# Kernel optimization log

Measured on AMD Instinct MI355X. Metric: run time of the kernel, lower is better.

## Reference

```python
import jax, jax.numpy as jnp
import numpy as np

EMBED_DIM = 1024
NUM_HEADS = 16
SEQ_LEN = 2048
BATCH = 2
LN_EPS = 1e-5


def setup_inputs() -> dict:
    key = jax.random.key(0)
    ks = jax.random.split(key, 12)
    d = EMBED_DIM
    s = 1.0 / np.sqrt(d)
    inp = {
        "x": jax.random.normal(ks[0], (BATCH, SEQ_LEN, d), dtype=jnp.float32),
        "ln1_g": jnp.ones((d,), jnp.float32),
        "ln1_b": jnp.zeros((d,), jnp.float32),
        "ln2_g": jnp.ones((d,), jnp.float32),
        "ln2_b": jnp.zeros((d,), jnp.float32),
        "W_qkv": jax.random.normal(ks[1], (d, 3 * d), jnp.float32) * s,
        "b_qkv": jnp.zeros((3 * d,), jnp.float32),
        "W_proj": jax.random.normal(ks[2], (d, d), jnp.float32) * s,
        "b_proj": jnp.zeros((d,), jnp.float32),
        "W_fc": jax.random.normal(ks[3], (d, 4 * d), jnp.float32) * s,
        "b_fc": jnp.zeros((4 * d,), jnp.float32),
        "W_out": jax.random.normal(ks[4], (4 * d, d), jnpp_dummy := jnp.float32) * (1.0 / np.sqrt(4 * d)),
        "b_out": jnp.zeros((d,), jnp.float32),
    }
    return inp


def _layernorm(x, g, b):
    mu = jnp.mean(x, axis=-1, keepdims=True)
    var = jnp.mean(jnp.square(x - mu), axis=-1, keepdims=True)
    return (x - mu) * jax.lax.rsqrt(var + LN_EPS) * g + b


def _block(x, ln1_g, ln1_b, ln2_g, ln2_b, W_qkv, b_qkv, W_proj, b_proj, W_fc, b_fc, W_out, b_out):
    B, S, D = x.shape
    H = NUM_HEADS
    hd = D // H
    h = _layernorm(x, ln1_g, ln1_b)
    qkv = h @ W_qkv + b_qkv  # [B,S,3D]
    q, k, v = jnp.split(qkv, 3, axis=-1)
    # [B,H,S,hd]
    q = q.reshape(B, S, H, hd).transpose(0, 2, 1, 3)
    k = k.reshape(B, S, H, hd).transpose(0, 2, 1, 3)
    v = v.reshape(B, S, H, hd).transpose(0, 2, 1, 3)
    attn = jnp.einsum("bhqd,bhkd->bhqk", q, k) / np.sqrt(hd).astype(np.float32)
    causal = jnp.tril(jnp.ones((S, S), dtype=bool))
    attn = jnp.where(causal, attn, -jnp.inf)
    attn = jax.nn.softmax(attn, axis=-1)
    y = jnp.einsum("bhqk,bhkd->bhqd", attn, v)
    y = y.transpose(0, 2, 1, 3).reshape(B, S, D)
    y = y @ W_proj + b_proj
    x = x + y
    h2 = _layernorm(x, ln2_g, ln2_b)
    m = jax.nn.relu(h2 @ W_fc + b_fc) @ W_out + b_out
    return x + m


def reference(x, ln1_g, ln1_b, ln2_g, ln2_b, W_qkv, b_qkv, W_proj, b_proj, W_fc, b_fc, W_out, b_out):
    return _block(x, ln1_g, ln1_b, ln2_g, ln2_b, W_qkv, b_qkv, W_proj, b_proj, W_fc, b_fc, W_out, b_out)
```

## Files before the change

kernel.cpp:

```cpp
#include <hip/hip_runtime.h>

typedef unsigned short u16;
typedef __attribute__((ext_vector_type(8))) __bf16 bf16x8;
typedef __attribute__((ext_vector_type(4))) float f32x4;

#define DEV __device__ __forceinline__

DEV u16 f2bf(float f) {
  unsigned u = __float_as_uint(f);
  u += 0x7fffu + ((u >> 16) & 1u);
  return (u16)(u >> 16);
}
DEV float bf2f(u16 u) { return __uint_as_float((unsigned)u << 16); }

DEV void gl_lds16(const void* g, void* l) {
  __builtin_amdgcn_global_load_lds(
      (const __attribute__((address_space(1))) void*)(uintptr_t)g,
      (__attribute__((address_space(3))) void*)(unsigned)(uintptr_t)l, 16, 0, 0);
}

DEV float wave_sum64(float v) {
#pragma unroll
  for (int off = 32; off > 0; off >>= 1) v += __shfl_down(v, off);
  return v;
}

DEV void ln_body(const float4 v, const float* g, const float* be, u16* out_row, int t,
                 float* red) {
  const int w = t >> 6, L = t & 63;
  float s = v.x + v.y + v.z + v.w;
  s = wave_sum64(s);
  if (L == 0) red[w] = s;
  __syncthreads();
  const float mean = (red[0] + red[1] + red[2] + red[3]) * (1.0f / 1024.0f);
  const float dx = v.x - mean, dy = v.y - mean, dz = v.z - mean, dw = v.w - mean;
  float q = dx * dx + dy * dy + dz * dz + dw * dw;
  q = wave_sum64(q);
  if (L == 0) red[4 + w] = q;
  __syncthreads();
  const float var = (red[4] + red[5] + red[6] + red[7]) * (1.0f / 1024.0f);
  const float rs = rsqrtf(var + 1e-5f);
  const float4 gg = reinterpret_cast<const float4*>(g)[t];
  const float4 bb = reinterpret_cast<const float4*>(be)[t];
  ushort4 o;
  o.x = f2bf(dx * rs * gg.x + bb.x);
  o.y = f2bf(dy * rs * gg.y + bb.y);
  o.z = f2bf(dz * rs * gg.z + bb.z);
  o.w = f2bf(dw * rs * gg.w + bb.w);
  reinterpret_cast<ushort4*>(out_row)[t] = o;
}

__global__ __launch_bounds__(256) void prep_kernel(
    const float* __restrict__ x, const float* __restrict__ ln1g,
    const float* __restrict__ ln1b, u16* __restrict__ hbuf,
    const float* __restrict__ Wqkv, u16* __restrict__ wt_qkv,
    const float* __restrict__ Wproj, u16* __restrict__ wt_proj,
    const float* __restrict__ Wfc, u16* __restrict__ wt_fc,
    const float* __restrict__ Wout, u16* __restrict__ wt_out) {
  __shared__ float smem[32 * 33];
  int id = blockIdx.x;
  const int t = threadIdx.x;
  if (id < 4096) {
    const float4 v = reinterpret_cast<const float4*>(x + (size_t)id * 1024)[t];
    ln_body(v, ln1g, ln1b, hbuf + (size_t)id * 1024, t, smem);
    return;
  }
  id -= 4096;
  const float* W;
  u16* Wt;
  int K, N, nbx;
  if (id < 3072) {
    W = Wqkv; Wt = wt_qkv; K = 1024; N = 3072; nbx = 96;
  } else if (id < 3072 + 1024) {
    id -= 3072; W = Wproj; Wt = wt_proj; K = 1024; N = 1024; nbx = 32;
  } else if (id < 3072 + 1024 + 4096) {
    id -= 3072 + 1024; W = Wfc; Wt = wt_fc; K = 1024; N = 4096; nbx = 128;
  } else {
    id -= 3072 + 1024 + 4096; W = Wout; Wt = wt_out; K = 4096; N = 1024; nbx = 32;
  }
  float(*tile)[33] = (float(*)[33])smem;
  const int c0 = (id % nbx) * 32, r0 = (id / nbx) * 32;
  const int tx = t & 31, ty = t >> 5;
#pragma unroll
  for (int j = 0; j < 4; ++j)
    tile[ty + j * 8][tx] = W[(size_t)(r0 + ty + j * 8) * N + c0 + tx];
  __syncthreads();
#pragma unroll
  for (int j = 0; j < 4; ++j) {
    const int n = c0 + ty + j * 8, k = r0 + tx;
    Wt[(size_t)n * K + k] = f2bf(tile[tx][ty + j * 8]);
  }
}

__global__ __launch_bounds__(256) void proj_reduce_ln(const float* __restrict__ x,
                                                      const float* __restrict__ bias,
                                                      const u16* __restrict__ P0,
                                                      const u16* __restrict__ P1,
                                                      const float* __restrict__ g,
                                                      const float* __restrict__ be,
                                                      float* __restrict__ x2,
                                                      u16* __restrict__ hbuf) {
  const int row = blockIdx.x, t = threadIdx.x;
  const size_t off = (size_t)row * 1024;
  __shared__ float red[8];
  const float4 xv = reinterpret_cast<const float4*>(x + off)[t];
  const float4 bv = reinterpret_cast<const float4*>(bias)[t];
  const ushort4 p0 = reinterpret_cast<const ushort4*>(P0 + off)[t];
  const ushort4 p1 = reinterpret_cast<const ushort4*>(P1 + off)[t];
  float4 v;
  v.x = xv.x + bv.x + bf2f(p0.x) + bf2f(p1.x);
  v.y = xv.y + bv.y + bf2f(p0.y) + bf2f(p1.y);
  v.z = xv.z + bv.z + bf2f(p0.z) + bf2f(p1.z);
  v.w = xv.w + bv.w + bf2f(p0.w) + bf2f(p1.w);
  reinterpret_cast<float4*>(x2 + off)[t] = v;
  ln_body(v, g, be, hbuf + off, t, red);
}

__global__ __launch_bounds__(256) void out_reduce(const float* __restrict__ x2,
                                                  const float* __restrict__ bias,
                                                  const u16* __restrict__ P0,
                                                  const u16* __restrict__ P1,
                                                  const u16* __restrict__ P2,
                                                  const u16* __restrict__ P3,
                                                  float* __restrict__ dout) {
  const int row = blockIdx.x, t = threadIdx.x;
  const size_t off = (size_t)row * 1024;
  const float4 xv = reinterpret_cast<const float4*>(x2 + off)[t];
  const float4 bv = reinterpret_cast<const float4*>(bias)[t];
  const ushort4 a = reinterpret_cast<const ushort4*>(P0 + off)[t];
  const ushort4 b = reinterpret_cast<const ushort4*>(P1 + off)[t];
  const ushort4 c = reinterpret_cast<const ushort4*>(P2 + off)[t];
  const ushort4 d = reinterpret_cast<const ushort4*>(P3 + off)[t];
  float4 o;
  o.x = xv.x + bv.x + bf2f(a.x) + bf2f(b.x) + bf2f(c.x) + bf2f(d.x);
  o.y = xv.y + bv.y + bf2f(a.y) + bf2f(b.y) + bf2f(c.y) + bf2f(d.y);
  o.z = xv.z + bv.z + bf2f(a.z) + bf2f(b.z) + bf2f(c.z) + bf2f(d.z);
  o.w = xv.w + bv.w + bf2f(a.w) + bf2f(b.w) + bf2f(c.w) + bf2f(d.w);
  reinterpret_cast<float4*>(dout + off)[t] = o;
}

enum { F_BIAS = 1, F_RESID = 2, F_RELU = 4, F_BF16 = 8, F_PART4 = 32, F_VT = 64 };

template <int FLAGS>
__global__ __launch_bounds__(256, 2) void gemm_bt(const u16* __restrict__ A,
                                                  const u16* __restrict__ Bt,
                                                  const float* __restrict__ bias,
                                                  const float* __restrict__ resid,
                                                  void* __restrict__ Cout,
                                                  u16* __restrict__ pp0, u16* __restrict__ pp1,
                                                  u16* __restrict__ pp2, u16* __restrict__ pp3,
                                                  int M, int N, int K, int Kst) {
  __shared__ __attribute__((aligned(16))) u16 sA[2][128 * 32];
  __shared__ __attribute__((aligned(16))) u16 sB[2][128 * 32];

  const int gx = gridDim.x, gy = gridDim.y;
  const int tilesPerZ = gx * gy;
  int lin = (blockIdx.z * gy + blockIdx.y) * gx + blockIdx.x;
  const int total = tilesPerZ * gridDim.z;
  if (!(total & 7)) lin = (lin & 7) * (total >> 3) + (lin >> 3);
  const int zz = lin / tilesPerZ;
  const int pid = lin - zz * tilesPerZ;
  const int npg = gx << 3;
  const int gid = pid / npg;
  const int rem = pid - gid * npg;
  const int fm = gid << 3;
  const int gsm = (gy - fm < 8) ? (gy - fm) : 8;
  const int bm = fm + rem % gsm;
  const int bn = rem / gsm;

  const int t = threadIdx.x, w = t >> 6, L = t & 63, quad = L >> 4, l15 = L & 15;
  const int wm = w >> 1, wn = w & 1;
  const int m0 = bm * 128, n0 = bn * 128;
  const u16* Ag = A + (size_t)m0 * Kst + (size_t)zz * K;
  const u16* Bg = Bt + (size_t)n0 * Kst + (size_t)zz * K;

  f32x4 acc[4][4] = {};

  for (int k0 = 0; k0 < K; k0 += 64) {
    __syncthreads();
#pragma unroll
    for (int h = 0; h < 2; ++h) {
#pragma unroll
      for (int i = 0; i < 2; ++i) {
        const int cp = i * 256 + t, rr = cp >> 2, cc = (cp & 3) << 3;
        gl_lds16(Ag + (size_t)rr * Kst + k0 + h * 32 + cc, &sA[h][(i * 256 + w * 64) * 8]);
      }
#pragma unroll
      for (int i = 0; i < 2; ++i) {
        const int cp = i * 256 + t, rr = cp >> 2, cc = (cp & 3) << 3;
        gl_lds16(Bg + (size_t)rr * Kst + k0 + h * 32 + cc, &sB[h][(i * 256 + w * 64) * 8]);
      }
    }
    __syncthreads();

#pragma unroll
    for (int h = 0; h < 2; ++h) {
      bf16x8 af[4], bfr[4];
#pragma unroll
      for (int m = 0; m < 4; ++m)
        af[m] = *(const bf16x8*)&sA[h][(wm * 64 + m * 16 + l15) * 32 + quad * 8];
#pragma unroll
      for (int n = 0; n < 4; ++n)
        bfr[n] = *(const bf16x8*)&sB[h][(wn * 64 + n * 16 + l15) * 32 + quad * 8];
#pragma unroll
      for (int m = 0; m < 4; ++m)
#pragma unroll
        for (int n = 0; n < 4; ++n)
          acc[m][n] =
              __builtin_amdgcn_mfma_f32_16x16x32_bf16(af[m], bfr[n], acc[m][n], 0, 0, 0);
    }
  }

  if ((FLAGS & F_VT) && n0 >= 2048) {
#pragma unroll
    for (int m = 0; m < 4; ++m) {
#pragma unroll
      for (int n = 0; n < 4; ++n) {
        const int col = n0 + wn * 64 + n * 16 + l15;
        const float bv = bias[col];
        const int hh = (col - 2048) >> 6, dd = col & 63;
        const int srow = m0 + wm * 64 + m * 16 + quad * 4;
        const int bb = srow >> 11, ss = srow & 2047;
        ushort4 tmp;
        tmp.x = f2bf(acc[m][n][0] + bv);
        tmp.y = f2bf(acc[m][n][1] + bv);
        tmp.z = f2bf(acc[m][n][2] + bv);
        tmp.w = f2bf(acc[m][n][3] + bv);
        *(ushort4*)(pp0 + ((size_t)((bb * 16 + hh) * 64 + dd)) * 2048 + ss) = tmp;
      }
    }
    return;
  }

  u16* pbase = nullptr;
  if (FLAGS & F_PART4)
    pbase = (zz == 0) ? pp0 : (zz == 1) ? pp1 : (zz == 2) ? pp2 : pp3;

#pragma unroll
  for (int m = 0; m < 4; ++m) {
#pragma unroll
    for (int n = 0; n < 4; ++n) {
      const int col = n0 + wn * 64 + n * 16 + l15;
      const float bv = (FLAGS & F_BIAS) ? bias[col] : 0.0f;
#pragma unroll
      for (int rr = 0; rr < 4; ++rr) {
        const int row = m0 + wm * 64 + m * 16 + quad * 4 + rr;
        if (FLAGS & F_PART4) {
          pbase[(size_t)row * N + col] = f2bf(acc[m][n][rr]);
        } else {
          float v = acc[m][n][rr] + bv;
          if (FLAGS & F_RESID) v += resid[(size_t)row * N + col];
          if (FLAGS & F_RELU) v = fmaxf(v, 0.0f);
          if (FLAGS & F_BF16)
            ((u16*)Cout)[(size_t)row * N + col] = f2bf(v);
          else
            ((float*)Cout)[(size_t)row * N + col] = v;
        }
      }
    }
  }
}

__global__ __launch_bounds__(512) void flash_attn(const u16* __restrict__ qkv,
                                                  const u16* __restrict__ Vt,
                                                  u16* __restrict__ y,
                                                  float* __restrict__ acc0,
                                                  float* __restrict__ acc1,
                                                  float* __restrict__ lacc0,
                                                  float* __restrict__ lacc1) {
  constexpr int S = 2048, D3 = 3072, D = 1024;
  constexpr float Csc = 0.125f * 1.44269504088896f;
  __shared__ __attribute__((aligned(16))) u16 sK[64 * 64];
  __shared__ __attribute__((aligned(16))) u16 sV[64 * 64];
  __shared__ __attribute__((aligned(16))) u16 sP[8][2 * 16 * 40];

  const int bid = blockIdx.x;
  const int bh = bid & 31;
  const int e = bid >> 5;
  int qt, it0, it1, part;
  if (e < 8) {
    qt = 8 + e; it0 = 0; it1 = 16; part = 1;
  } else {
    const int j = (e - 8) >> 1;
    if (((e - 8) & 1) == 0) {
      qt = 7 - j; it0 = 0; it1 = 2 * qt + 2; part = 0;
    } else {
      qt = 15 - j; it0 = 16; it1 = 2 * qt + 2; part = 2;
    }
  }
  const int b = bh >> 4, h = bh & 15;
  const int q0 = qt * 128;

  const int t = threadIdx.x, w = t >> 6, L = t & 63, quad = L >> 4, l15 = L & 15;
  const int qw = q0 + w * 16;

  const u16* qbase = qkv + (size_t)(b * S) * D3 + h * 64;
  const u16* Kbase = qbase + D;
  const u16* Vbase = Vt + (size_t)((b * 16 + h) * 64) * S;

  const int srow = t >> 3;
  const int k8 = ((t & 7) ^ (srow & 7)) << 3;
  const u16* Ksrc = Kbase + (size_t)srow * D3 + k8;
  const u16* Vsrc = Vbase + (size_t)srow * S + k8;
  u16* sKdst = &sK[(w * 64) * 8];
  u16* sVdst = &sV[(w * 64) * 8];

  bf16x8 aQ[2];
#pragma unroll
  for (int kk = 0; kk < 2; ++kk)
    aQ[kk] = *(const bf16x8*)(qbase + (size_t)(qw + l15) * D3 + kk * 32 + quad * 8);

  bf16x8 ones;
#pragma unroll
  for (int i = 0; i < 8; ++i) ones[i] = (__bf16)1.0f;

  f32x4 acc[4] = {};
  f32x4 lacc = {};

  u16* sPw = sP[w];
  const int swz = l15 & 7;

  gl_lds16(Ksrc + (size_t)(it0 * 64) * D3, sKdst);
  gl_lds16(Vsrc + it0 * 64, sVdst);

  for (int it = it0; it < it1; ++it) {
    const int kv0 = it * 64;
    asm volatile("s_waitcnt vmcnt(0)" ::: "memory");
    __builtin_amdgcn_s_barrier();

    f32x4 s[4] = {};
    __builtin_amdgcn_s_setprio(1);
#pragma unroll
    for (int kk = 0; kk < 2; ++kk) {
#pragma unroll
      for (int n = 0; n < 4; ++n) {
        const bf16x8 bK =
            *(const bf16x8*)&sK[(n * 16 + l15) * 64 + ((kk * 4 + quad) ^ swz) * 8];
        s[n] = __builtin_amdgcn_mfma_f32_16x16x32_bf16(aQ[kk], bK, s[n], 0, 0, 0);
      }
    }
    __builtin_amdgcn_s_setprio(0);

    if (kv0 + 63 > qw) {
#pragma unroll
      for (int n = 0; n < 4; ++n) {
        const int col = kv0 + n * 16 + l15;
#pragma unroll
        for (int r = 0; r < 4; ++r) {
          const int row = qw + quad * 4 + r;
          const float p = __builtin_amdgcn_exp2f(s[n][r] * Csc);
          s[n][r] = (col > row) ? 0.0f : p;
        }
      }
    } else {
#pragma unroll
      for (int n = 0; n < 4; ++n)
#pragma unroll
        for (int r = 0; r < 4; ++r) s[n][r] = __builtin_amdgcn_exp2f(s[n][r] * Csc);
    }

#pragma unroll
    for (int n = 0; n < 4; ++n)
#pragma unroll
      for (int r = 0; r < 4; ++r)
        sPw[(n >> 1) * 640 + (quad * 4 + r) * 40 + (n & 1) * 16 + l15] = f2bf(s[n][r]);

    __builtin_amdgcn_s_setprio(1);
#pragma unroll
    for (int kk = 0; kk < 2; ++kk) {
      const bf16x8 aP = *(const bf16x8*)&sPw[kk * 640 + l15 * 40 + quad * 8];
      lacc = __builtin_amdgcn_mfma_f32_16x16x32_bf16(aP, ones, lacc, 0, 0, 0);
#pragma unroll
      for (int dn = 0; dn < 4; ++dn) {
        const bf16x8 bV =
            *(const bf16x8*)&sV[(dn * 16 + l15) * 64 + ((kk * 4 + quad) ^ swz) * 8];
        acc[dn] = __builtin_amdgcn_mfma_f32_16x16x32_bf16(aP, bV, acc[dn], 0, 0, 0);
      }
    }
    __builtin_amdgcn_s_setprio(0);

    asm volatile("s_waitcnt lgkmcnt(0)" ::: "memory");
    __builtin_amdgcn_s_barrier();
    if (it + 1 < it1) {
      const int kvn = kv0 + 64;
      gl_lds16(Ksrc + (size_t)kvn * D3, sKdst);
      gl_lds16(Vsrc + kvn, sVdst);
    }
  }

  if (part == 0) {
#pragma unroll
    for (int r = 0; r < 4; ++r) {
      const float inv = 1.0f / lacc[r];
      const int row = qw + quad * 4 + r;
      u16* yb = y + (size_t)(b * S + row) * D + h * 64 + l15;
#pragma unroll
      for (int dn = 0; dn < 4; ++dn) yb[dn * 16] = f2bf(acc[dn][r] * inv);
    }
  } else {
    float* accP = (part == 1) ? acc0 : acc1;
    float* laccP = (part == 1) ? lacc0 : lacc1;
#pragma unroll
    for (int r = 0; r < 4; ++r) {
      const int row = qw + quad * 4 + r;
      const int g = (bh << 10) + (row - 1024);
      float* ap = accP + (size_t)g * 64 + l15;
#pragma unroll
      for (int dn = 0; dn < 4; ++dn) ap[dn * 16] = acc[dn][r];
      if (l15 == 0) laccP[g] = lacc[r];
    }
  }
}

__global__ __launch_bounds__(256) void attn_combine(const float* __restrict__ acc0,
                                                    const float* __restrict__ acc1,
                                                    const float* __restrict__ lacc0,
                                                    const float* __restrict__ lacc1,
                                                    u16* __restrict__ y) {
  const int t = threadIdx.x;
  const int g = blockIdx.x * 4 + (t >> 6);
  const int d = t & 63;
  const int bh = g >> 10, ri = g & 1023;
  const int b = bh >> 4, h = bh & 15;
  const int row = 1024 + ri;
  const size_t po = (size_t)g * 64 + d;
  const float l = lacc0[g] + lacc1[g];
  const float v = (acc0[po] + acc1[po]) / l;
  y[((size_t)(b * 2048 + row)) * 1024 + h * 64 + d] = f2bf(v);
}

extern "C" void kernel_launch(void* const* d_in, const int* in_sizes, int n_in,
                              void* d_out, int out_size, void* d_ws, size_t ws_size,
                              hipStream_t stream) {
  const float* x = (const float*)d_in[0];
  const float* ln1g = (const float*)d_in[1];
  const float* ln1b = (const float*)d_in[2];
  const float* ln2g = (const float*)d_in[3];
  const float* ln2b = (const float*)d_in[4];
  const float* Wqkv = (const float*)d_in[5];
  const float* bqkv = (const float*)d_in[6];
  const float* Wproj = (const float*)d_in[7];
  const float* bproj = (const float*)d_in[8];
  const float* Wfc = (const float*)d_in[9];
  const float* bfc = (const float*)d_in[10];
  const float* Wout = (const float*)d_in[11];
  const float* bout = (const float*)d_in[12];

  char* ws = (char*)d_ws;
  const size_t MB = 1u << 20;
  u16* wt_out = (u16*)(ws + 0 * MB);
  u16* hbuf = (u16*)(ws + 8 * MB);
  float* x2 = (float*)(ws + 16 * MB);
  u16* ybuf = (u16*)(ws + 32 * MB);
  u16* qkvb = (u16*)(ws + 40 * MB);
  u16* vtb = (u16*)(ws + 64 * MB);
  u16* wt_qkv = (u16*)(ws + 72 * MB);
  u16* wt_proj = (u16*)(ws + 78 * MB);
  u16* wt_fc = (u16*)(ws + 80 * MB);
  u16* projP0 = (u16*)(ws + 40 * MB);
  u16* projP1 = (u16*)(ws + 48 * MB);
  u16* m1 = (u16*)(ws + 40 * MB);
  u16* po0 = (u16*)(ws + 8 * MB);
  u16* po1 = (u16*)(ws + 32 * MB);
  u16* po2 = (u16*)(ws + 72 * MB);
  u16* po3 = (u16*)(ws + 80 * MB);
  float* facc0 = (float*)(ws + 8 * MB);
  float* facc1 = (float*)(ws + 16 * MB);
  float* flacc0 = (float*)(ws + 24 * MB);
  float* flacc1 = (float*)(ws + 25 * MB);

  prep_kernel<<<4096 + 3072 + 1024 + 4096 + 4096, 256, 0, stream>>>(
      x, ln1g, ln1b, hbuf, Wqkv, wt_qkv, Wproj, wt_proj, Wfc, wt_fc, Wout, wt_out);

  gemm_bt<F_BIAS | F_BF16 | F_VT><<<dim3(24, 32), 256, 0, stream>>>(
      hbuf, wt_qkv, bqkv, nullptr, qkvb, vtb, nullptr, nullptr, nullptr,
      4096, 3072, 1024, 1024);
  flash_attn<<<768, 512, 0, stream>>>(qkvb, vtb, ybuf, facc0, facc1, flacc0, flacc1);
  attn_combine<<<8192, 256, 0, stream>>>(facc0, facc1, flacc0, flacc1, ybuf);

  gemm_bt<F_PART4><<<dim3(8, 32, 2), 256, 0, stream>>>(
      ybuf, wt_proj, nullptr, nullptr, nullptr, projP0, projP1, nullptr, nullptr,
      4096, 1024, 512, 1024);
  proj_reduce_ln<<<4096, 256, 0, stream>>>(x, bproj, projP0, projP1, ln2g, ln2b, x2, hbuf);

  gemm_bt<F_BIAS | F_RELU | F_BF16><<<dim3(32, 32), 256, 0, stream>>>(
      hbuf, wt_fc, bfc, nullptr, m1, nullptr, nullptr, nullptr, nullptr,
      4096, 4096, 1024, 1024);

  gemm_bt<F_PART4><<<dim3(8, 32, 4), 256, 0, stream>>>(
      m1, wt_out, nullptr, nullptr, nullptr, po0, po1, po2, po3,
      4096, 1024, 1024, 4096);
  out_reduce<<<4096, 256, 0, stream>>>(x2, bout, po0, po1, po2, po3, (float*)d_out);
}
```

Baseline: 315.1 us.

## Fuse attention split-K combine into flash kernel and halve out-GEMM K split

Removes the separate attn_combine kernel. The flash attention blocks handling the two halves of a split row tile now use an atomic counter: the last block to finish reads the other half's partial accumulator and sum, normalizes, and writes bf16 output. Flags are zeroed inside prep_kernel. Separately, the output projection GEMM drops from a 4-way to a 2-way K split, cutting partial-buffer traffic and out_reduce loads but giving fewer blocks and longer K loops per block. The counter relies on threadfence ordering between the two blocks.

Result: slower. 493.5 us (+56.6%).

```diff
diff --git a/kernel.cpp b/kernel.cpp
--- a/kernel.cpp
+++ b/kernel.cpp
@@ -56,10 +56,12 @@
     const float* __restrict__ Wqkv, u16* __restrict__ wt_qkv,
     const float* __restrict__ Wproj, u16* __restrict__ wt_proj,
     const float* __restrict__ Wfc, u16* __restrict__ wt_fc,
-    const float* __restrict__ Wout, u16* __restrict__ wt_out) {
+    const float* __restrict__ Wout, u16* __restrict__ wt_out,
+    int* __restrict__ flags) {
   __shared__ float smem[32 * 33];
   int id = blockIdx.x;
   const int t = threadIdx.x;
+  if (id == 4096) flags[t] = 0;
   if (id < 4096) {
     const float4 v = reinterpret_cast<const float4*>(x + (size_t)id * 1024)[t];
     ln_body(v, ln1g, ln1b, hbuf + (size_t)id * 1024, t, smem);
@@ -120,8 +122,6 @@
                                                   const float* __restrict__ bias,
                                                   const u16* __restrict__ P0,
                                                   const u16* __restrict__ P1,
-                                                  const u16* __restrict__ P2,
-                                                  const u16* __restrict__ P3,
                                                   float* __restrict__ dout) {
   const int row = blockIdx.x, t = threadIdx.x;
   const size_t off = (size_t)row * 1024;
@@ -129,13 +129,11 @@
   const float4 bv = reinterpret_cast<const float4*>(bias)[t];
   const ushort4 a = reinterpret_cast<const ushort4*>(P0 + off)[t];
   const ushort4 b = reinterpret_cast<const ushort4*>(P1 + off)[t];
-  const ushort4 c = reinterpret_cast<const ushort4*>(P2 + off)[t];
-  const ushort4 d = reinterpret_cast<const ushort4*>(P3 + off)[t];
   float4 o;
-  o.x = xv.x + bv.x + bf2f(a.x) + bf2f(b.x) + bf2f(c.x) + bf2f(d.x);
-  o.y = xv.y + bv.y + bf2f(a.y) + bf2f(b.y) + bf2f(c.y) + bf2f(d.y);
-  o.z = xv.z + bv.z + bf2f(a.z) + bf2f(b.z) + bf2f(c.z) + bf2f(d.z);
-  o.w = xv.w + bv.w + bf2f(a.w) + bf2f(b.w) + bf2f(c.w) + bf2f(d.w);
+  o.x = xv.x + bv.x + bf2f(a.x) + bf2f(b.x);
+  o.y = xv.y + bv.y + bf2f(a.y) + bf2f(b.y);
+  o.z = xv.z + bv.z + bf2f(a.z) + bf2f(b.z);
+  o.w = xv.w + bv.w + bf2f(a.w) + bf2f(b.w);
   reinterpret_cast<float4*>(dout + off)[t] = o;
 }
 
@@ -267,12 +265,14 @@
                                                   float* __restrict__ acc0,
                                                   float* __restrict__ acc1,
                                                   float* __restrict__ lacc0,
-                                                  float* __restrict__ lacc1) {
+                                                  float* __restrict__ lacc1,
+                                                  int* __restrict__ flags) {
   constexpr int S = 2048, D3 = 3072, D = 1024;
   constexpr float Csc = 0.125f * 1.44269504088896f;
   __shared__ __attribute__((aligned(16))) u16 sK[64 * 64];
   __shared__ __attribute__((aligned(16))) u16 sV[64 * 64];
   __shared__ __attribute__((aligned(16))) u16 sP[8][2 * 16 * 40];
+  __shared__ int s_old;
 
   const int bid = blockIdx.x;
   const int bh = bid & 31;
@@ -397,36 +397,40 @@
 #pragma unroll
       for (int dn = 0; dn < 4; ++dn) yb[dn * 16] = f2bf(acc[dn][r] * inv);
     }
-  } else {
-    float* accP = (part == 1) ? acc0 : acc1;
-    float* laccP = (part == 1) ? lacc0 : lacc1;
+    return;
+  }
+
+  float* accP = (part == 1) ? acc0 : acc1;
+  float* laccP = (part == 1) ? lacc0 : lacc1;
+#pragma unroll
+  for (int r = 0; r < 4; ++r) {
+    const int row = qw + quad * 4 + r;
+    const int g = (bh << 10) + (row - 1024);
+    float* ap = accP + (size_t)g * 64 + l15;
+#pragma unroll
+    for (int dn = 0; dn < 4; ++dn) ap[dn * 16] = acc[dn][r];
+    if (l15 == 0) laccP[g] = lacc[r];
+  }
+  __threadfence();
+  __syncthreads();
+  if (t == 0) s_old = atomicAdd(&flags[((qt - 8) << 5) | bh], 1);
+  __syncthreads();
+  if (s_old == 1) {
+    __threadfence();
+    const float* accO = (part == 1) ? acc1 : acc0;
+    const float* laccO = (part == 1) ? lacc1 : lacc0;
 #pragma unroll
     for (int r = 0; r < 4; ++r) {
       const int row = qw + quad * 4 + r;
       const int g = (bh << 10) + (row - 1024);
-      float* ap = accP + (size_t)g * 64 + l15;
-#pragma unroll
-      for (int dn = 0; dn < 4; ++dn) ap[dn * 16] = acc[dn][r];
-      if (l15 == 0) laccP[g] = lacc[r];
-    }
-  }
-}
-
-__global__ __launch_bounds__(256) void attn_combine(const float* __restrict__ acc0,
-                                                    const float* __restrict__ acc1,
-                                                    const float* __restrict__ lacc0,
-                                                    const float* __restrict__ lacc1,
-                                                    u16* __restrict__ y) {
-  const int t = threadIdx.x;
-  const int g = blockIdx.x * 4 + (t >> 6);
-  const int d = t & 63;
-  const int bh = g >> 10, ri = g & 1023;
-  const int b = bh >> 4, h = bh & 15;
-  const int row = 1024 + ri;
-  const size_t po = (size_t)g * 64 + d;
-  const float l = lacc0[g] + lacc1[g];
-  const float v = (acc0[po] + acc1[po]) / l;
-  y[((size_t)(b * 2048 + row)) * 1024 + h * 64 + d] = f2bf(v);
+      const float inv = 1.0f / (lacc[r] + laccO[g]);
+      const float* ao = accO + (size_t)g * 64 + l15;
+      u16* yb = y + (size_t)(b * S + row) * D + h * 64 + l15;
+#pragma unroll
+      for (int dn = 0; dn < 4; ++dn)
+        yb[dn * 16] = f2bf((acc[dn][r] + ao[dn * 16]) * inv);
+    }
+  }
 }
 
 extern "C" void kernel_launch(void* const* d_in, const int* in_sizes, int n_in,
@@ -462,21 +466,21 @@
   u16* m1 = (u16*)(ws + 40 * MB);
   u16* po0 = (u16*)(ws + 8 * MB);
   u16* po1 = (u16*)(ws + 32 * MB);
-  u16* po2 = (u16*)(ws + 72 * MB);
-  u16* po3 = (u16*)(ws + 80 * MB);
   float* facc0 = (float*)(ws + 8 * MB);
   float* facc1 = (float*)(ws + 16 * MB);
   float* flacc0 = (float*)(ws + 24 * MB);
   float* flacc1 = (float*)(ws + 25 * MB);
+  int* fflags = (int*)(ws + 26 * MB);
 
   prep_kernel<<<4096 + 3072 + 1024 + 4096 + 4096, 256, 0, stream>>>(
-      x, ln1g, ln1b, hbuf, Wqkv, wt_qkv, Wproj, wt_proj, Wfc, wt_fc, Wout, wt_out);
+      x, ln1g, ln1b, hbuf, Wqkv, wt_qkv, Wproj, wt_proj, Wfc, wt_fc, Wout, wt_out,
+      fflags);
 
   gemm_bt<F_BIAS | F_BF16 | F_VT><<<dim3(24, 32), 256, 0, stream>>>(
       hbuf, wt_qkv, bqkv, nullptr, qkvb, vtb, nullptr, nullptr, nullptr,
       4096, 3072, 1024, 1024);
-  flash_attn<<<768, 512, 0, stream>>>(qkvb, vtb, ybuf, facc0, facc1, flacc0, flacc1);
-  attn_combine<<<8192, 256, 0, stream>>>(facc0, facc1, flacc0, flacc1, ybuf);
+  flash_attn<<<768, 512, 0, stream>>>(qkvb, vtb, ybuf, facc0, facc1, flacc0, flacc1,
+                                      fflags);
 
   gemm_bt<F_PART4><<<dim3(8, 32, 2), 256, 0, stream>>>(
       ybuf, wt_proj, nullptr, nullptr, nullptr, projP0, projP1, nullptr, nullptr,
@@ -487,8 +491,8 @@
       hbuf, wt_fc, bfc, nullptr, m1, nullptr, nullptr, nullptr, nullptr,
       4096, 4096, 1024, 1024);
 
-  gemm_bt<F_PART4><<<dim3(8, 32, 4), 256, 0, stream>>>(
-      m1, wt_out, nullptr, nullptr, nullptr, po0, po1, po2, po3,
-      4096, 1024, 1024, 4096);
-  out_reduce<<<4096, 256, 0, stream>>>(x2, bout, po0, po1, po2, po3, (float*)d_out);
-}
+  gemm_bt<F_PART4><<<dim3(8, 32, 2), 256, 0, stream>>>(
+      m1, wt_out, nullptr, nullptr, nullptr, po0, po1, nullptr, nullptr,
+      4096, 1024, 2048, 4096);
+  out_reduce<<<4096, 256, 0, stream>>>(x2, bout, po0, po1, (float*)d_out);
+}
```
